# Performance work log

Hardware: AMD Instinct MI355X
Metric: run time of the kernel (lower is better)

Reference implementation:

```python
import jax, jax.numpy as jnp
import numpy as np

N, DEG, IN_DIM, HID, OUT = 50000, 32, 256, 256, 128

def setup_inputs() -> dict:
    key = jax.random.key(0)
    k1, k2, k3, k4, k5, k6 = jax.random.split(key, 6)
    node_features = jax.random.normal(k1, (N, IN_DIM), dtype=jnp.float32)
    neighbor_idx = jax.random.randint(k2, (N, DEG), 0, N)
    scale1 = 1.0 / np.sqrt(2 * IN_DIM)
    scale2 = 1.0 / np.sqrt(HID)
    W1 = jax.random.normal(k3, (HID, 2 * IN_DIM), dtype=jnp.float32) * scale1
    b1 = jax.random.normal(k4, (HID,), dtype=jnp.float32) * scale1
    W2 = jax.random.normal(k5, (OUT, HID), dtype=jnp.float32) * scale2
    b2 = jax.random.normal(k6, (OUT,), dtype=jnp.float32) * scale2
    return {"node_features": node_features, "neighbor_idx": neighbor_idx,
            "W1": W1, "b1": b1, "W2": W2, "b2": b2}

def reference(node_features, neighbor_idx, W1, b1, W2, b2):
    # Layer 0 (mean aggregator, with neighbors):
    # gather [N, DEG, IN_DIM] neighbor features, mean over DEG
    nbr_mean = jnp.mean(node_features[neighbor_idx], axis=1)  # [N, IN_DIM]
    combined = jnp.concatenate([node_features, nbr_mean], axis=-1)  # [N, 2*IN_DIM]
    h = jax.nn.relu(combined @ W1.T + b1)  # [N, HID]
    # Layer 1: empty neighbor list -> linear_without_neighbors + relu
    out = jax.nn.relu(h @ W2.T + b2)  # [N, OUT]
    return out
```

## Files before the change

### kernel.cpp

```cpp
#include <hip/hip_runtime.h>
#include <stdint.h>

#define N_NODES 50000
#define DEG     32
#define IN_DIM  256
#define K1      512
#define HID     256
#define OUT_DIM 128

#define NCHUNK  4
#define CDIM    64
#define SLICE8  ((size_t)N_NODES * CDIM)
#define GT      16

#define MT     32
#define NTILES ((N_NODES + MT - 1) / MT)
#define GBLK   256
#define CSTR   520
#define HSTR   264

typedef __bf16 bf16x8 __attribute__((ext_vector_type(8)));
typedef float  f32x4  __attribute__((ext_vector_type(4)));
typedef float  f32x2  __attribute__((ext_vector_type(2)));

#define PIN(x) asm volatile("" : "+v"(x))

__device__ __forceinline__ unsigned short f2bf(float f) {
    union { float f; unsigned u; } v; v.f = f;
    unsigned r = v.u + 0x7fffu + ((v.u >> 16) & 1u);
    return (unsigned short)(r >> 16);
}
__device__ __forceinline__ int clampN(int v) {
    return v < 0 ? 0 : (v >= N_NODES ? N_NODES - 1 : v);
}
__device__ __forceinline__ void async_copy16(const void* g, void* l) {
    __builtin_amdgcn_global_load_lds(
        (const __attribute__((address_space(1))) void*)g,
        (__attribute__((address_space(3))) void*)l, 16, 0, 0);
}

#define FEAT_BLKS ((N_NODES + 7) / 8)
__global__ __launch_bounds__(256)
void prep_all(const float* __restrict__ feat,
              const float* __restrict__ W1, const float* __restrict__ W2,
              const int*   __restrict__ nbr,
              unsigned short* __restrict__ featb,
              unsigned char*  __restrict__ featF8,
              unsigned short* __restrict__ W1b, unsigned short* __restrict__ W2b,
              unsigned short* __restrict__ nbr16)
{
    const int t = threadIdx.x;
    if (blockIdx.x < FEAT_BLKS) {
        const int node = blockIdx.x * 8 + (t >> 5);
        const int seg  = t & 31;
        if (node < N_NODES) {
            const float4* src = (const float4*)(feat + (size_t)node * IN_DIM + seg * 8);
            float4 f0 = src[0], f1 = src[1];
            ushort4 o0, o1;
            o0.x = f2bf(f0.x); o0.y = f2bf(f0.y); o0.z = f2bf(f0.z); o0.w = f2bf(f0.w);
            o1.x = f2bf(f1.x); o1.y = f2bf(f1.y); o1.z = f2bf(f1.z); o1.w = f2bf(f1.w);
            unsigned short* db = featb + (size_t)node * IN_DIM + seg * 8;
            *(ushort4*)db       = o0;
            *(ushort4*)(db + 4) = o1;
            int u0 = 0, u1 = 0;
            u0 = __builtin_amdgcn_cvt_pk_fp8_f32(f0.x, f0.y, u0, false);
            u0 = __builtin_amdgcn_cvt_pk_fp8_f32(f0.z, f0.w, u0, true);
            u1 = __builtin_amdgcn_cvt_pk_fp8_f32(f1.x, f1.y, u1, false);
            u1 = __builtin_amdgcn_cvt_pk_fp8_f32(f1.z, f1.w, u1, true);
            const int c   = seg >> 3;
            const int off = (seg & 7) * 8;
            unsigned char* d8 = featF8 + (size_t)c * SLICE8 + (size_t)node * CDIM + off;
            ((int*)d8)[0] = u0;
            ((int*)d8)[1] = u1;
        }
    } else {
        const int bid = blockIdx.x - FEAT_BLKS;
        const int stride = 256 * 256 * 4;
        const int tid4 = (bid * 256 + t) * 4;
        for (int i = tid4; i < HID * K1; i += stride) {
            float4 f = *(const float4*)(W1 + i);
            ushort4 o; o.x = f2bf(f.x); o.y = f2bf(f.y); o.z = f2bf(f.z); o.w = f2bf(f.w);
            *(ushort4*)(W1b + i) = o;
        }
        for (int i = tid4; i < OUT_DIM * HID; i += stride) {
            float4 f = *(const float4*)(W2 + i);
            ushort4 o; o.x = f2bf(f.x); o.y = f2bf(f.y); o.z = f2bf(f.z); o.w = f2bf(f.w);
            *(ushort4*)(W2b + i) = o;
        }
        for (int i = tid4; i < N_NODES * DEG; i += stride) {
            int4 v = *(const int4*)(nbr + i);
            ushort4 o;
            o.x = (unsigned short)clampN(v.x); o.y = (unsigned short)clampN(v.y);
            o.z = (unsigned short)clampN(v.z); o.w = (unsigned short)clampN(v.w);
            *(ushort4*)(nbr16 + i) = o;
        }
    }
}

__global__ __launch_bounds__(128)
void gather_mean_fp8(const unsigned char*  __restrict__ featF8,
                     const unsigned short* __restrict__ nbr16,
                     unsigned short*       __restrict__ meanb)
{
    __shared__ unsigned short sIdx[GT * DEG];
    const int tid  = threadIdx.x;
    const int c    = blockIdx.y;
    const int base = blockIdx.x * GT;

    *(ushort4*)(sIdx + tid * 4) =
        *(const ushort4*)(nbr16 + (size_t)base * DEG + tid * 4);
    __syncthreads();

    const unsigned char* slice = featF8 + (size_t)c * SLICE8;
    const int grp = tid >> 3;
    const int ln  = tid & 7;
    const unsigned short* idxr = sIdx + grp * DEG;

    uint2 vv[DEG];
    #pragma unroll
    for (int j = 0; j < DEG; ++j) {
        int nb = idxr[j];
        vv[j] = *(const uint2*)(slice + (size_t)nb * CDIM + ln * 8);
    }
    float s[8];
    #pragma unroll
    for (int k = 0; k < 8; ++k) s[k] = 0.f;
    #pragma unroll
    for (int j = 0; j < DEG; ++j) {
        f32x2 a = __builtin_amdgcn_cvt_pk_f32_fp8(vv[j].x, false);
        f32x2 b = __builtin_amdgcn_cvt_pk_f32_fp8(vv[j].x, true);
        f32x2 d = __builtin_amdgcn_cvt_pk_f32_fp8(vv[j].y, false);
        f32x2 e = __builtin_amdgcn_cvt_pk_f32_fp8(vv[j].y, true);
        s[0] += a[0]; s[1] += a[1]; s[2] += b[0]; s[3] += b[1];
        s[4] += d[0]; s[5] += d[1]; s[6] += e[0]; s[7] += e[1];
    }
    const float sc = 1.0f / 32.0f;
    ushort4 o0, o1;
    o0.x = f2bf(s[0] * sc); o0.y = f2bf(s[1] * sc);
    o0.z = f2bf(s[2] * sc); o0.w = f2bf(s[3] * sc);
    o1.x = f2bf(s[4] * sc); o1.y = f2bf(s[5] * sc);
    o1.z = f2bf(s[6] * sc); o1.w = f2bf(s[7] * sc);
    unsigned short* dst = meanb + (size_t)(base + grp) * IN_DIM + c * CDIM + ln * 8;
    *(ushort4*)dst       = o0;
    *(ushort4*)(dst + 4) = o1;
}

__global__ __launch_bounds__(512, 2)
void sage_gemm_pipe(const unsigned short* __restrict__ featb,
                    const unsigned short* __restrict__ meanb,
                    const unsigned short* __restrict__ W1b,
                    const float*          __restrict__ b1,
                    const unsigned short* __restrict__ W2b,
                    const float*          __restrict__ b2,
                    float*                __restrict__ out)
{
    __shared__ __align__(16) unsigned short sC[2][MT * CSTR];
    __shared__ __align__(16) unsigned short sH[2][MT * HSTR];

    const int tid  = threadIdx.x;
    const int lane = tid & 63;
    const int wave = tid >> 6;
    const int r    = lane & 15;
    const int q    = lane >> 4;

    bf16x8 w1f[2][16];
    #pragma unroll
    for (int nt = 0; nt < 2; ++nt) {
        const size_t nrow = (size_t)(wave * 32 + nt * 16 + r) * K1;
        #pragma unroll
        for (int kk = 0; kk < 16; ++kk) {
            w1f[nt][kk] = *(const bf16x8*)(W1b + nrow + kk * 32 + q * 8);
            PIN(w1f[nt][kk]);
        }
    }
    bf16x8 w2f[8];
    {
        const size_t orow = (size_t)(wave * 16 + r) * HID;
        #pragma unroll
        for (int kk = 0; kk < 8; ++kk) {
            w2f[kk] = *(const bf16x8*)(W2b + orow + kk * 32 + q * 8);
            PIN(w2f[kk]);
        }
    }
    const float4 bias1v0 = *(const float4*)(b1 + wave * 32 + q * 4);
    const float4 bias1v1 = *(const float4*)(b1 + wave * 32 + 16 + q * 4);
    const float4 bias2v  = *(const float4*)(b2 + wave * 16 + q * 4);

    auto stage = [&](int tile, int buf) {
        const int tbase = tile * MT;
        #pragma unroll
        for (int j = 0; j < 4; ++j) {
            const int i = wave * 4 + j;
            int node = tbase + i;
            if (node >= N_NODES) node = N_NODES - 1;
            const unsigned short* g = (lane < 32)
                ? featb + (size_t)node * IN_DIM + lane * 8
                : meanb + (size_t)node * IN_DIM + (lane - 32) * 8;
            async_copy16(g, &sC[buf][i * CSTR]);
        }
    };

    auto phase2 = [&](int cbuf, int hbuf) {
        f32x4 acc[2][2];
        #pragma unroll
        for (int mt = 0; mt < 2; ++mt)
            #pragma unroll
            for (int nt = 0; nt < 2; ++nt)
                acc[mt][nt] = (f32x4){0.f, 0.f, 0.f, 0.f};
        #pragma unroll
        for (int kk = 0; kk < 16; ++kk) {
            bf16x8 a0 = *(const bf16x8*)(&sC[cbuf][r * CSTR + kk * 32 + q * 8]);
            bf16x8 a1 = *(const bf16x8*)(&sC[cbuf][(16 + r) * CSTR + kk * 32 + q * 8]);
            acc[0][0] = __builtin_amdgcn_mfma_f32_16x16x32_bf16(w1f[0][kk], a0, acc[0][0], 0, 0, 0);
            acc[1][0] = __builtin_amdgcn_mfma_f32_16x16x32_bf16(w1f[0][kk], a1, acc[1][0], 0, 0, 0);
            acc[0][1] = __builtin_amdgcn_mfma_f32_16x16x32_bf16(w1f[1][kk], a0, acc[0][1], 0, 0, 0);
            acc[1][1] = __builtin_amdgcn_mfma_f32_16x16x32_bf16(w1f[1][kk], a1, acc[1][1], 0, 0, 0);
        }
        #pragma unroll
        for (int nt = 0; nt < 2; ++nt) {
            const float4 bias = nt ? bias1v1 : bias1v0;
            #pragma unroll
            for (int mt = 0; mt < 2; ++mt) {
                float v0 = acc[mt][nt][0] + bias.x;
                float v1 = acc[mt][nt][1] + bias.y;
                float v2 = acc[mt][nt][2] + bias.z;
                float v3 = acc[mt][nt][3] + bias.w;
                ushort4 o;
                o.x = f2bf(v0 > 0.f ? v0 : 0.f);
                o.y = f2bf(v1 > 0.f ? v1 : 0.f);
                o.z = f2bf(v2 > 0.f ? v2 : 0.f);
                o.w = f2bf(v3 > 0.f ? v3 : 0.f);
                *(ushort4*)(&sH[hbuf][(mt * 16 + r) * HSTR + wave * 32 + nt * 16 + q * 4]) = o;
            }
        }
    };

    auto phase3 = [&](int hbuf, int pbase) {
        f32x4 acc3[2];
        acc3[0] = (f32x4){0.f, 0.f, 0.f, 0.f};
        acc3[1] = (f32x4){0.f, 0.f, 0.f, 0.f};
        #pragma unroll
        for (int kk = 0; kk < 8; ++kk) {
            bf16x8 h0 = *(const bf16x8*)(&sH[hbuf][r * HSTR + kk * 32 + q * 8]);
            bf16x8 h1 = *(const bf16x8*)(&sH[hbuf][(16 + r) * HSTR + kk * 32 + q * 8]);
            acc3[0] = __builtin_amdgcn_mfma_f32_16x16x32_bf16(w2f[kk], h0, acc3[0], 0, 0, 0);
            acc3[1] = __builtin_amdgcn_mfma_f32_16x16x32_bf16(w2f[kk], h1, acc3[1], 0, 0, 0);
        }
        #pragma unroll
        for (int mt = 0; mt < 2; ++mt) {
            const int node = pbase + mt * 16 + r;
            if (node < N_NODES) {
                float4 v;
                v.x = acc3[mt][0] + bias2v.x; v.x = v.x > 0.f ? v.x : 0.f;
                v.y = acc3[mt][1] + bias2v.y; v.y = v.y > 0.f ? v.y : 0.f;
                v.z = acc3[mt][2] + bias2v.z; v.z = v.z > 0.f ? v.z : 0.f;
                v.w = acc3[mt][3] + bias2v.w; v.w = v.w > 0.f ? v.w : 0.f;
                *(float4*)(out + (size_t)node * OUT_DIM + wave * 16 + q * 4) = v;
            }
        }
    };

    int tile = blockIdx.x;
    int buf = 0, hb = 0;
    int prev_base = -1;
    if (tile < NTILES) stage(tile, 0);

    for (; tile < NTILES; tile += GBLK) {
        __syncthreads();
        if (tile + GBLK < NTILES) stage(tile + GBLK, buf ^ 1);
        phase2(buf, hb);
        if (prev_base >= 0) phase3(hb ^ 1, prev_base);
        prev_base = tile * MT;
        buf ^= 1; hb ^= 1;
    }
    __syncthreads();
    if (prev_base >= 0) phase3(hb ^ 1, prev_base);
}

__global__ __launch_bounds__(256)
void sage_naive(const float* __restrict__ feat, const int* __restrict__ nbr,
                const float* __restrict__ W1, const float* __restrict__ b1,
                const float* __restrict__ W2, const float* __restrict__ b2,
                float* __restrict__ out) {
    __shared__ float comb[K1];
    __shared__ float h[HID];
    const int node = blockIdx.x;
    const int t = threadIdx.x;
    comb[t] = feat[(size_t)node * IN_DIM + t];
    float acc = 0.f;
    for (int d = 0; d < DEG; ++d) {
        int nb = clampN(nbr[node * DEG + d]);
        acc += feat[(size_t)nb * IN_DIM + t];
    }
    comb[IN_DIM + t] = acc * (1.0f / 32.0f);
    __syncthreads();
    float s = b1[t];
    for (int k = 0; k < K1; ++k) s += comb[k] * W1[(size_t)t * K1 + k];
    h[t] = s > 0.f ? s : 0.f;
    __syncthreads();
    if (t < OUT_DIM) {
        float s2 = b2[t];
        for (int k = 0; k < HID; ++k) s2 += h[k] * W2[(size_t)t * HID + k];
        out[(size_t)node * OUT_DIM + t] = s2 > 0.f ? s2 : 0.f;
    }
}

extern "C" void kernel_launch(void* const* d_in, const int* in_sizes, int n_in,
                              void* d_out, int out_size, void* d_ws, size_t ws_size,
                              hipStream_t stream) {
    const float* feat = (const float*)d_in[0];
    const int*   nbr  = (const int*)d_in[1];
    const float* W1   = (const float*)d_in[2];
    const float* b1   = (const float*)d_in[3];
    const float* W2   = (const float*)d_in[4];
    const float* b2   = (const float*)d_in[5];
    float* out = (float*)d_out;

    const size_t feat_elems = (size_t)N_NODES * IN_DIM;
    const size_t w1_elems   = (size_t)HID * K1;
    const size_t w2_elems   = (size_t)OUT_DIM * HID;
    const size_t mean_elems = (size_t)N_NODES * IN_DIM;
    const size_t idx_elems  = (size_t)N_NODES * DEG;
    const size_t u16_elems  = feat_elems + w1_elems + w2_elems + mean_elems + idx_elems;
    const size_t need = u16_elems * sizeof(unsigned short)
                      + (size_t)NCHUNK * SLICE8;

    if (ws_size >= need) {
        unsigned short* featb  = (unsigned short*)d_ws;
        unsigned short* W1b    = featb + feat_elems;
        unsigned short* W2b    = W1b + w1_elems;
        unsigned short* meanb  = W2b + w2_elems;
        unsigned short* nbr16  = meanb + mean_elems;
        unsigned char*  featF8 = (unsigned char*)(nbr16 + idx_elems);

        prep_all<<<FEAT_BLKS + 256, 256, 0, stream>>>(feat, W1, W2, nbr,
                                                      featb, featF8, W1b, W2b, nbr16);
        gather_mean_fp8<<<dim3(N_NODES / GT, NCHUNK), 128, 0, stream>>>(featF8, nbr16, meanb);
        sage_gemm_pipe<<<GBLK, 512, 0, stream>>>(featb, meanb, W1b, b1, W2b, b2, out);
    } else {
        sage_naive<<<N_NODES, 256, 0, stream>>>(feat, nbr, W1, b1, W2, b2, out);
    }
}
```

Baseline: 177.2 us.

## Load GEMM A operands straight from global memory instead of LDS staging

Removes the double-buffered async global-to-LDS staging of the combined feature/mean tile and the software-pipelined phase2/phase3 overlap. Each wave now loads its bf16 A fragments directly from global memory, runs the layer-1 MFMAs, syncs, then runs layer 2 on the same tile. This frees a large LDS buffer and drops the staging, but every wave re-reads the same rows from global/L2 (8x redundant across waves) and loses the prefetch overlap across tiles.

Result: slower. 214.7 us (+21.2%).

```diff
diff --git a/kernel.cpp b/kernel.cpp
--- a/kernel.cpp
+++ b/kernel.cpp
@@ -16,7 +16,6 @@
 #define MT     32
 #define NTILES ((N_NODES + MT - 1) / MT)
 #define GBLK   256
-#define CSTR   520
 #define HSTR   264
 
 typedef __bf16 bf16x8 __attribute__((ext_vector_type(8)));
@@ -32,11 +31,6 @@
 }
 __device__ __forceinline__ int clampN(int v) {
     return v < 0 ? 0 : (v >= N_NODES ? N_NODES - 1 : v);
-}
-__device__ __forceinline__ void async_copy16(const void* g, void* l) {
-    __builtin_amdgcn_global_load_lds(
-        (const __attribute__((address_space(1))) void*)g,
-        (__attribute__((address_space(3))) void*)l, 16, 0, 0);
 }
 
 #define FEAT_BLKS ((N_NODES + 7) / 8)
@@ -146,15 +140,14 @@
 }
 
 __global__ __launch_bounds__(512, 2)
-void sage_gemm_pipe(const unsigned short* __restrict__ featb,
-                    const unsigned short* __restrict__ meanb,
-                    const unsigned short* __restrict__ W1b,
-                    const float*          __restrict__ b1,
-                    const unsigned short* __restrict__ W2b,
-                    const float*          __restrict__ b2,
-                    float*                __restrict__ out)
+void sage_gemm_direct(const unsigned short* __restrict__ featb,
+                      const unsigned short* __restrict__ meanb,
+                      const unsigned short* __restrict__ W1b,
+                      const float*          __restrict__ b1,
+                      const unsigned short* __restrict__ W2b,
+                      const float*          __restrict__ b2,
+                      float*                __restrict__ out)
 {
-    __shared__ __align__(16) unsigned short sC[2][MT * CSTR];
     __shared__ __align__(16) unsigned short sH[2][MT * HSTR];
 
     const int tid  = threadIdx.x;
@@ -186,35 +179,40 @@
     const float4 bias1v1 = *(const float4*)(b1 + wave * 32 + 16 + q * 4);
     const float4 bias2v  = *(const float4*)(b2 + wave * 16 + q * 4);
 
-    auto stage = [&](int tile, int buf) {
+    int hb = 0;
+    for (int tile = blockIdx.x; tile < NTILES; tile += GBLK) {
         const int tbase = tile * MT;
-        #pragma unroll
-        for (int j = 0; j < 4; ++j) {
-            const int i = wave * 4 + j;
-            int node = tbase + i;
-            if (node >= N_NODES) node = N_NODES - 1;
-            const unsigned short* g = (lane < 32)
-                ? featb + (size_t)node * IN_DIM + lane * 8
-                : meanb + (size_t)node * IN_DIM + (lane - 32) * 8;
-            async_copy16(g, &sC[buf][i * CSTR]);
-        }
-    };
-
-    auto phase2 = [&](int cbuf, int hbuf) {
+        int n0 = tbase + r;      if (n0 > N_NODES - 1) n0 = N_NODES - 1;
+        int n1 = tbase + 16 + r; if (n1 > N_NODES - 1) n1 = N_NODES - 1;
+        const unsigned short* f0 = featb + (size_t)n0 * IN_DIM + q * 8;
+        const unsigned short* f1 = featb + (size_t)n1 * IN_DIM + q * 8;
+        const unsigned short* m0 = meanb + (size_t)n0 * IN_DIM + q * 8;
+        const unsigned short* m1 = meanb + (size_t)n1 * IN_DIM + q * 8;
+
         f32x4 acc[2][2];
         #pragma unroll
         for (int mt = 0; mt < 2; ++mt)
             #pragma unroll
             for (int nt = 0; nt < 2; ++nt)
                 acc[mt][nt] = (f32x4){0.f, 0.f, 0.f, 0.f};
-        #pragma unroll
-        for (int kk = 0; kk < 16; ++kk) {
-            bf16x8 a0 = *(const bf16x8*)(&sC[cbuf][r * CSTR + kk * 32 + q * 8]);
-            bf16x8 a1 = *(const bf16x8*)(&sC[cbuf][(16 + r) * CSTR + kk * 32 + q * 8]);
+
+        #pragma unroll
+        for (int kk = 0; kk < 8; ++kk) {
+            bf16x8 a0 = *(const bf16x8*)(f0 + kk * 32);
+            bf16x8 a1 = *(const bf16x8*)(f1 + kk * 32);
             acc[0][0] = __builtin_amdgcn_mfma_f32_16x16x32_bf16(w1f[0][kk], a0, acc[0][0], 0, 0, 0);
             acc[1][0] = __builtin_amdgcn_mfma_f32_16x16x32_bf16(w1f[0][kk], a1, acc[1][0], 0, 0, 0);
             acc[0][1] = __builtin_amdgcn_mfma_f32_16x16x32_bf16(w1f[1][kk], a0, acc[0][1], 0, 0, 0);
             acc[1][1] = __builtin_amdgcn_mfma_f32_16x16x32_bf16(w1f[1][kk], a1, acc[1][1], 0, 0, 0);
+        }
+        #pragma unroll
+        for (int kk = 0; kk < 8; ++kk) {
+            bf16x8 a0 = *(const bf16x8*)(m0 + kk * 32);
+            bf16x8 a1 = *(const bf16x8*)(m1 + kk * 32);
+            acc[0][0] = __builtin_amdgcn_mfma_f32_16x16x32_bf16(w1f[0][8 + kk], a0, acc[0][0], 0, 0, 0);
+            acc[1][0] = __builtin_amdgcn_mfma_f32_16x16x32_bf16(w1f[0][8 + kk], a1, acc[1][0], 0, 0, 0);
+            acc[0][1] = __builtin_amdgcn_mfma_f32_16x16x32_bf16(w1f[1][8 + kk], a0, acc[0][1], 0, 0, 0);
+            acc[1][1] = __builtin_amdgcn_mfma_f32_16x16x32_bf16(w1f[1][8 + kk], a1, acc[1][1], 0, 0, 0);
         }
         #pragma unroll
         for (int nt = 0; nt < 2; ++nt) {
@@ -230,51 +228,37 @@
                 o.y = f2bf(v1 > 0.f ? v1 : 0.f);
                 o.z = f2bf(v2 > 0.f ? v2 : 0.f);
                 o.w = f2bf(v3 > 0.f ? v3 : 0.f);
-                *(ushort4*)(&sH[hbuf][(mt * 16 + r) * HSTR + wave * 32 + nt * 16 + q * 4]) = o;
+                *(ushort4*)(&sH[hb][(mt * 16 + r) * HSTR + wave * 32 + nt * 16 + q * 4]) = o;
             }
         }
-    };
-
-    auto phase3 = [&](int hbuf, int pbase) {
-        f32x4 acc3[2];
-        acc3[0] = (f32x4){0.f, 0.f, 0.f, 0.f};
-        acc3[1] = (f32x4){0.f, 0.f, 0.f, 0.f};
-        #pragma unroll
-        for (int kk = 0; kk < 8; ++kk) {
-            bf16x8 h0 = *(const bf16x8*)(&sH[hbuf][r * HSTR + kk * 32 + q * 8]);
-            bf16x8 h1 = *(const bf16x8*)(&sH[hbuf][(16 + r) * HSTR + kk * 32 + q * 8]);
-            acc3[0] = __builtin_amdgcn_mfma_f32_16x16x32_bf16(w2f[kk], h0, acc3[0], 0, 0, 0);
-            acc3[1] = __builtin_amdgcn_mfma_f32_16x16x32_bf16(w2f[kk], h1, acc3[1], 0, 0, 0);
-        }
-        #pragma unroll
-        for (int mt = 0; mt < 2; ++mt) {
-            const int node = pbase + mt * 16 + r;
-            if (node < N_NODES) {
-                float4 v;
-                v.x = acc3[mt][0] + bias2v.x; v.x = v.x > 0.f ? v.x : 0.f;
-                v.y = acc3[mt][1] + bias2v.y; v.y = v.y > 0.f ? v.y : 0.f;
-                v.z = acc3[mt][2] + bias2v.z; v.z = v.z > 0.f ? v.z : 0.f;
-                v.w = acc3[mt][3] + bias2v.w; v.w = v.w > 0.f ? v.w : 0.f;
-                *(float4*)(out + (size_t)node * OUT_DIM + wave * 16 + q * 4) = v;
+        __syncthreads();
+
+        {
+            f32x4 acc3[2];
+            acc3[0] = (f32x4){0.f, 0.f, 0.f, 0.f};
+            acc3[1] = (f32x4){0.f, 0.f, 0.f, 0.f};
+            #pragma unroll
+            for (int kk = 0; kk < 8; ++kk) {
+                bf16x8 h0 = *(const bf16x8*)(&sH[hb][r * HSTR + kk * 32 + q * 8]);
+                bf16x8 h1 = *(const bf16x8*)(&sH[hb][(16 + r) * HSTR + kk * 32 + q * 8]);
+                acc3[0] = __builtin_amdgcn_mfma_f32_16x16x32_bf16(w2f[kk], h0, acc3[0], 0, 0, 0);
+                acc3[1] = __builtin_amdgcn_mfma_f32_16x16x32_bf16(w2f[kk], h1, acc3[1], 0, 0, 0);
             }
-        }
-    };
-
-    int tile = blockIdx.x;
-    int buf = 0, hb = 0;
-    int prev_base = -1;
-    if (tile < NTILES) stage(tile, 0);
-
-    for (; tile < NTILES; tile += GBLK) {
-        __syncthreads();
-        if (tile + GBLK < NTILES) stage(tile + GBLK, buf ^ 1);
-        phase2(buf, hb);
-        if (prev_base >= 0) phase3(hb ^ 1, prev_base);
-        prev_base = tile * MT;
-        buf ^= 1; hb ^= 1;
-    }
-    __syncthreads();
-    if (prev_base >= 0) phase3(hb ^ 1, prev_base);
+            #pragma unroll
+            for (int mt = 0; mt < 2; ++mt) {
+                const int node = tbase + mt * 16 + r;
+                if (node < N_NODES) {
+                    float4 v;
+                    v.x = acc3[mt][0] + bias2v.x; v.x = v.x > 0.f ? v.x : 0.f;
+                    v.y = acc3[mt][1] + bias2v.y; v.y = v.y > 0.f ? v.y : 0.f;
+                    v.z = acc3[mt][2] + bias2v.z; v.z = v.z > 0.f ? v.z : 0.f;
+                    v.w = acc3[mt][3] + bias2v.w; v.w = v.w > 0.f ? v.w : 0.f;
+                    *(float4*)(out + (size_t)node * OUT_DIM + wave * 16 + q * 4) = v;
+                }
+            }
+        }
+        hb ^= 1;
+    }
 }
 
 __global__ __launch_bounds__(256)
@@ -336,7 +320,7 @@
         prep_all<<<FEAT_BLKS + 256, 256, 0, stream>>>(feat, W1, W2, nbr,
                                                       featb, featF8, W1b, W2b, nbr16);
         gather_mean_fp8<<<dim3(N_NODES / GT, NCHUNK), 128, 0, stream>>>(featF8, nbr16, meanb);
-        sage_gemm_pipe<<<GBLK, 512, 0, stream>>>(featb, meanb, W1b, b1, W2b, b2, out);
+        sage_gemm_direct<<<GBLK, 512, 0, stream>>>(featb, meanb, W1b, b1, W2b, b2, out);
     } else {
         sage_naive<<<N_NODES, 256, 0, stream>>>(feat, nbr, W1, b1, W2, b2, out);
     }
```

## Halve GEMM block to 4 waves, each holding twice the weight fragments

Applied to the files above, without the earlier changes.

The fused two-layer GEMM kernel now runs 256 threads (4 waves) per block instead of 512. Each wave keeps 64 W1 output columns and 32 W2 output columns in registers (up to 512 VGPRs with launch bounds 256,1) rather than 32 and 16. The aim is to cut the number of waves that load the same staged activation tile from LDS and to issue more MFMAs per LDS read. In exchange, occupancy drops to one block of four waves per CU, so there is less latency hiding, and register pressure rises sharply with a risk of spills.

After: 186.9 us. 1.05x slower.

```diff
diff --git a/kernel.cpp b/kernel.cpp
--- a/kernel.cpp
+++ b/kernel.cpp
@@ -145,8 +145,8 @@
     *(ushort4*)(dst + 4) = o1;
 }
 
-__global__ __launch_bounds__(512, 2)
-void sage_gemm_pipe(const unsigned short* __restrict__ featb,
+__global__ __launch_bounds__(256, 1)
+void sage_gemm_r512(const unsigned short* __restrict__ featb,
                     const unsigned short* __restrict__ meanb,
                     const unsigned short* __restrict__ W1b,
                     const float*          __restrict__ b1,
@@ -163,34 +163,39 @@
     const int r    = lane & 15;
     const int q    = lane >> 4;
 
-    bf16x8 w1f[2][16];
-    #pragma unroll
-    for (int nt = 0; nt < 2; ++nt) {
-        const size_t nrow = (size_t)(wave * 32 + nt * 16 + r) * K1;
+    bf16x8 w1f[4][16];
+    #pragma unroll
+    for (int nt = 0; nt < 4; ++nt) {
+        const size_t nrow = (size_t)(wave * 64 + nt * 16 + r) * K1;
         #pragma unroll
         for (int kk = 0; kk < 16; ++kk) {
             w1f[nt][kk] = *(const bf16x8*)(W1b + nrow + kk * 32 + q * 8);
             PIN(w1f[nt][kk]);
         }
     }
-    bf16x8 w2f[8];
-    {
-        const size_t orow = (size_t)(wave * 16 + r) * HID;
+    bf16x8 w2f[2][8];
+    #pragma unroll
+    for (int nt = 0; nt < 2; ++nt) {
+        const size_t orow = (size_t)(wave * 32 + nt * 16 + r) * HID;
         #pragma unroll
         for (int kk = 0; kk < 8; ++kk) {
-            w2f[kk] = *(const bf16x8*)(W2b + orow + kk * 32 + q * 8);
-            PIN(w2f[kk]);
-        }
-    }
-    const float4 bias1v0 = *(const float4*)(b1 + wave * 32 + q * 4);
-    const float4 bias1v1 = *(const float4*)(b1 + wave * 32 + 16 + q * 4);
-    const float4 bias2v  = *(const float4*)(b2 + wave * 16 + q * 4);
+            w2f[nt][kk] = *(const bf16x8*)(W2b + orow + kk * 32 + q * 8);
+            PIN(w2f[nt][kk]);
+        }
+    }
+    float4 bias1v[4], bias2v[2];
+    #pragma unroll
+    for (int nt = 0; nt < 4; ++nt)
+        bias1v[nt] = *(const float4*)(b1 + wave * 64 + nt * 16 + q * 4);
+    #pragma unroll
+    for (int nt = 0; nt < 2; ++nt)
+        bias2v[nt] = *(const float4*)(b2 + wave * 32 + nt * 16 + q * 4);
 
     auto stage = [&](int tile, int buf) {
         const int tbase = tile * MT;
         #pragma unroll
-        for (int j = 0; j < 4; ++j) {
-            const int i = wave * 4 + j;
+        for (int j = 0; j < 8; ++j) {
+            const int i = wave * 8 + j;
             int node = tbase + i;
             if (node >= N_NODES) node = N_NODES - 1;
             const unsigned short* g = (lane < 32)
@@ -201,24 +206,25 @@
     };
 
     auto phase2 = [&](int cbuf, int hbuf) {
-        f32x4 acc[2][2];
+        f32x4 acc[2][4];
         #pragma unroll
         for (int mt = 0; mt < 2; ++mt)
             #pragma unroll
-            for (int nt = 0; nt < 2; ++nt)
+            for (int nt = 0; nt < 4; ++nt)
                 acc[mt][nt] = (f32x4){0.f, 0.f, 0.f, 0.f};
         #pragma unroll
         for (int kk = 0; kk < 16; ++kk) {
             bf16x8 a0 = *(const bf16x8*)(&sC[cbuf][r * CSTR + kk * 32 + q * 8]);
             bf16x8 a1 = *(const bf16x8*)(&sC[cbuf][(16 + r) * CSTR + kk * 32 + q * 8]);
-            acc[0][0] = __builtin_amdgcn_mfma_f32_16x16x32_bf16(w1f[0][kk], a0, acc[0][0], 0, 0, 0);
-            acc[1][0] = __builtin_amdgcn_mfma_f32_16x16x32_bf16(w1f[0][kk], a1, acc[1][0], 0, 0, 0);
-            acc[0][1] = __builtin_amdgcn_mfma_f32_16x16x32_bf16(w1f[1][kk], a0, acc[0][1], 0, 0, 0);
-            acc[1][1] = __builtin_amdgcn_mfma_f32_16x16x32_bf16(w1f[1][kk], a1, acc[1][1], 0, 0, 0);
-        }
-        #pragma unroll
-        for (int nt = 0; nt < 2; ++nt) {
-            const float4 bias = nt ? bias1v1 : bias1v0;
+            #pragma unroll
+            for (int nt = 0; nt < 4; ++nt) {
+                acc[0][nt] = __builtin_amdgcn_mfma_f32_16x16x32_bf16(w1f[nt][kk], a0, acc[0][nt], 0, 0, 0);
+                acc[1][nt] = __builtin_amdgcn_mfma_f32_16x16x32_bf16(w1f[nt][kk], a1, acc[1][nt], 0, 0, 0);
+            }
+        }
+        #pragma unroll
+        for (int nt = 0; nt < 4; ++nt) {
+            const float4 bias = bias1v[nt];
             #pragma unroll
             for (int mt = 0; mt < 2; ++mt) {
                 float v0 = acc[mt][nt][0] + bias.x;
@@ -230,32 +236,41 @@
                 o.y = f2bf(v1 > 0.f ? v1 : 0.f);
                 o.z = f2bf(v2 > 0.f ? v2 : 0.f);
                 o.w = f2bf(v3 > 0.f ? v3 : 0.f);
-                *(ushort4*)(&sH[hbuf][(mt * 16 + r) * HSTR + wave * 32 + nt * 16 + q * 4]) = o;
+                *(ushort4*)(&sH[hbuf][(mt * 16 + r) * HSTR + wave * 64 + nt * 16 + q * 4]) = o;
             }
         }
     };
 
     auto phase3 = [&](int hbuf, int pbase) {
-        f32x4 acc3[2];
-        acc3[0] = (f32x4){0.f, 0.f, 0.f, 0.f};
-        acc3[1] = (f32x4){0.f, 0.f, 0.f, 0.f};
+        f32x4 acc3[2][2];
+        #pragma unroll
+        for (int mt = 0; mt < 2; ++mt)
+            #pragma unroll
+            for (int nt = 0; nt < 2; ++nt)
+                acc3[mt][nt] = (f32x4){0.f, 0.f, 0.f, 0.f};
         #pragma unroll
         for (int kk = 0; kk < 8; ++kk) {
             bf16x8 h0 = *(const bf16x8*)(&sH[hbuf][r * HSTR + kk * 32 + q * 8]);
             bf16x8 h1 = *(const bf16x8*)(&sH[hbuf][(16 + r) * HSTR + kk * 32 + q * 8]);
-            acc3[0] = __builtin_amdgcn_mfma_f32_16x16x32_bf16(w2f[kk], h0, acc3[0], 0, 0, 0);
-            acc3[1] = __builtin_amdgcn_mfma_f32_16x16x32_bf16(w2f[kk], h1, acc3[1], 0, 0, 0);
+            #pragma unroll
+            for (int nt = 0; nt < 2; ++nt) {
+                acc3[0][nt] = __builtin_amdgcn_mfma_f32_16x16x32_bf16(w2f[nt][kk], h0, acc3[0][nt], 0, 0, 0);
+                acc3[1][nt] = __builtin_amdgcn_mfma_f32_16x16x32_bf16(w2f[nt][kk], h1, acc3[1][nt], 0, 0, 0);
+            }
         }
         #pragma unroll
         for (int mt = 0; mt < 2; ++mt) {
             const int node = pbase + mt * 16 + r;
             if (node < N_NODES) {
-                float4 v;
-                v.x = acc3[mt][0] + bias2v.x; v.x = v.x > 0.f ? v.x : 0.f;
-                v.y = acc3[mt][1] + bias2v.y; v.y = v.y > 0.f ? v.y : 0.f;
-                v.z = acc3[mt][2] + bias2v.z; v.z = v.z > 0.f ? v.z : 0.f;
-                v.w = acc3[mt][3] + bias2v.w; v.w = v.w > 0.f ? v.w : 0.f;
-                *(float4*)(out + (size_t)node * OUT_DIM + wave * 16 + q * 4) = v;
+                #pragma unroll
+                for (int nt = 0; nt < 2; ++nt) {
+                    float4 v;
+                    v.x = acc3[mt][nt][0] + bias2v[nt].x; v.x = v.x > 0.f ? v.x : 0.f;
+                    v.y = acc3[mt][nt][1] + bias2v[nt].y; v.y = v.y > 0.f ? v.y : 0.f;
+                    v.z = acc3[mt][nt][2] + bias2v[nt].z; v.z = v.z > 0.f ? v.z : 0.f;
+                    v.w = acc3[mt][nt][3] + bias2v[nt].w; v.w = v.w > 0.f ? v.w : 0.f;
+                    *(float4*)(out + (size_t)node * OUT_DIM + wave * 32 + nt * 16 + q * 4) = v;
+                }
             }
         }
     };
@@ -336,7 +351,7 @@
         prep_all<<<FEAT_BLKS + 256, 256, 0, stream>>>(feat, W1, W2, nbr,
                                                       featb, featF8, W1b, W2b, nbr16);
         gather_mean_fp8<<<dim3(N_NODES / GT, NCHUNK), 128, 0, stream>>>(featF8, nbr16, meanb);
-        sage_gemm_pipe<<<GBLK, 512, 0, stream>>>(featb, meanb, W1b, b1, W2b, b2, out);
+        sage_gemm_r512<<<GBLK, 256, 0, stream>>>(featb, meanb, W1b, b1, W2b, b2, out);
     } else {
         sage_naive<<<N_NODES, 256, 0, stream>>>(feat, nbr, W1, b1, W2, b2, out);
     }
```
